# Kernel tuning notes

Measured on AMD Instinct MI355X. Metric: run time of the kernel, lower is better.

Reference implementation:

```python
import jax, jax.numpy as jnp
import numpy as np

N = 200_000
E = 6_400_000
EPS = 1e-12


def l2_normalize(x):
    # F.normalize(x, p=2, dim=1): x / max(||x||_2, eps)
    n = jnp.linalg.norm(x, axis=1, keepdims=True)
    return x / jnp.maximum(n, EPS)


def gcn_conv(x, W, b, src, dst, n):
    """PyG GCNConv: add self-loops, symmetric normalization D^-1/2 A D^-1/2,
    linear transform (no bias) on nodes, scatter-add to targets, then + bias."""
    loop = jnp.arange(n)
    s = jnp.concatenate([src, loop])  # sources (messages gathered here)
    d = jnp.concatenate([dst, loop])  # targets (aggregation here)
    deg = jax.ops.segment_sum(jnp.ones(s.shape[0], dtype=x.dtype), d, num_segments=n)
    dinv = jnp.where(deg > 0, jax.lax.rsqrt(deg), 0.0)
    norm = dinv[s] * dinv[d]  # [E+N]
    h = x @ W  # [N, out]
    out = jax.ops.segment_sum(norm[:, None] * h[s], d, num_segments=n)
    return out + b


def setup_inputs() -> dict:
    key = jax.random.key(0)
    ks = jax.random.split(key, 10)
    x = jax.random.normal(ks[0], (N, 3), dtype=jnp.float32)
    edge_index = jax.random.randint(ks[1], (2, E), 0, N, dtype=jnp.int64)

    def glorot(k, shape):
        lim = float(np.sqrt(6.0 / (shape[0] + shape[1])))
        return jax.random.uniform(k, shape, jnp.float32, -lim, lim)

    return {
        "x": x,
        "edge_index": edge_index,
        "W1": glorot(ks[2], (3, 6)),   "b1": jnp.zeros((6,), jnp.float32),
        "W2": glorot(ks[3], (6, 12)),  "b2": jnp.zeros((12,), jnp.float32),
        "W3": glorot(ks[4], (12, 24)), "b3": jnp.zeros((24,), jnp.float32),
        "Wc": glorot(ks[5], (24, 13)), "bc": jnp.zeros((13,), jnp.float32),
    }


def reference(x, edge_index, W1, b1, W2, b2, W3, b3, Wc, bc):
    src, dst = edge_index[0], edge_index[1]
    n = x.shape[0]
    h = jnp.tanh(gcn_conv(x, W1, b1, src, dst, n))
    h = jnp.tanh(l2_normalize(gcn_conv(h, W2, b2, src, dst, n)))
    h = l2_normalize(gcn_conv(h, W3, b3, src, dst, n))
    h = h @ Wc + bc
    return l2_normalize(h)
```

## Files before the change

### kernel.cpp

```cpp
#include <hip/hip_runtime.h>
#include <math.h>


static constexpr int NN = 200000;
static constexpr int NE = 6400000;
static constexpr int BK = 256;

static constexpr int SUBW  = 512;
static constexpr int NBA   = (NN + SUBW - 1) / SUBW;
static constexpr int CAP   = 32;
static constexpr int FLUSH = 16;
static constexpr int CAPB  = 18400;
static constexpr int BKP   = 512;
static constexpr int EPT   = 4;
static constexpr int CHUNK = BKP * EPT;
static constexpr int GPART = 768;
static constexpr int SRCSH = 13;
static constexpr int NSB   = (NN + (1 << SRCSH) - 1) >> SRCSH;

static constexpr int S     = 4;
static constexpr int LOGS  = 2;

__global__ void __launch_bounds__(BKP) k_part(const int* __restrict__ srcI,
                                              const int* __restrict__ dstI,
                                              unsigned* __restrict__ stg,
                                              int* __restrict__ gtail, int e) {
  __shared__ unsigned bin[CAP][NBA];
  __shared__ int bcnt[NBA];
  for (int t = threadIdx.x; t < NBA; t += BKP) bcnt[t] = 0;
  __syncthreads();
  int nchunks = (e + CHUNK - 1) / CHUNK;
  for (int c = blockIdx.x; c < nchunks; c += gridDim.x) {
    int base_i = c * CHUNK;
    int dv[EPT], sv[EPT];
#pragma unroll
    for (int u = 0; u < EPT; ++u) {
      int i = base_i + u * BKP + (int)threadIdx.x;
      dv[u] = (i < e) ? __builtin_nontemporal_load(dstI + i) : -1;
      sv[u] = (i < e) ? __builtin_nontemporal_load(srcI + i) : 0;
    }
#pragma unroll
    for (int u = 0; u < EPT; ++u) {
      if (dv[u] >= 0) {
        int b = dv[u] >> 9;
        unsigned rec = ((unsigned)(dv[u] & (SUBW - 1)) << 18) | (unsigned)sv[u];
        int p = atomicAdd(&bcnt[b], 1);
        if (p < CAP) {
          bin[p][b] = rec;
        } else {
          int base = atomicAdd(&gtail[b], 1);
          stg[(size_t)b * CAPB + base] = rec;
        }
      }
    }
    __syncthreads();
    int b2 = threadIdx.x;
    if (b2 < NBA) {
      int c2 = bcnt[b2];
      if (c2 > CAP) c2 = CAP;
      if (c2 >= FLUSH) {
        int nfl = c2 & ~(FLUSH - 1);
        int base = atomicAdd(&gtail[b2], nfl);
        size_t o = (size_t)b2 * CAPB + base;
        for (int k = 0; k < nfl; k += 4) {
          uint4 v;
          v.x = bin[k][b2]; v.y = bin[k + 1][b2]; v.z = bin[k + 2][b2]; v.w = bin[k + 3][b2];
          *(uint4*)(stg + o + k) = v;
        }
        int r = c2 - nfl;
        for (int k = 0; k < r; ++k) bin[k][b2] = bin[nfl + k][b2];
        bcnt[b2] = r;
      }
    }
    __syncthreads();
  }
  int b2 = threadIdx.x;
  if (b2 < NBA) {
    int c2 = bcnt[b2];
    if (c2 > CAP) c2 = CAP;
    if (c2 > 0) {
      int base = atomicAdd(&gtail[b2], c2);
      size_t o = (size_t)b2 * CAPB + base;
      for (int k = 0; k < c2; ++k) stg[o + k] = bin[k][b2];
    }
  }
}

__global__ void k_scan_sub(const int* __restrict__ gtail, int* __restrict__ sbase) {
  __shared__ int s0[512], s1[512];
  int t = threadIdx.x;
  int v = (t < NBA) ? gtail[t] : 0;
  s0[t] = v;
  __syncthreads();
  int* a = s0; int* b = s1;
  for (int off = 1; off < 512; off <<= 1) {
    int x = a[t] + ((t >= off) ? a[t - off] : 0);
    b[t] = x;
    __syncthreads();
    int* tmp = a; a = b; b = tmp;
  }
  if (t < NBA) sbase[t] = a[t] - v;
}

__global__ void __launch_bounds__(BK) k_build(const unsigned* __restrict__ stg,
                                              const int* __restrict__ gtail,
                                              const int* __restrict__ sbase,
                                              int* __restrict__ rowptr,
                                              int* __restrict__ adj,
                                              int* __restrict__ b7,
                                              int* __restrict__ b13,
                                              int* __restrict__ b19) {
  __shared__ unsigned hist2[SUBW * NSB];
  __shared__ int htot[SUBW];
  __shared__ int s0[SUBW], s1[SUBW];
  int b = blockIdx.x;
  int m = gtail[b]; if (m > CAPB) m = CAPB;
  size_t off = (size_t)b * CAPB;
  int base = sbase[b];
  if (b == NBA - 1 && threadIdx.x == 0) rowptr[NN] = base + m;
  for (int t = threadIdx.x; t < SUBW * NSB; t += BK) hist2[t] = 0;
  __syncthreads();
  for (int k = threadIdx.x; k < m; k += BK) {
    unsigned rec = stg[off + k];
    int dl = rec >> 18;
    int sb = (int)((rec & 0x3FFFFu) >> SRCSH);
    atomicAdd(&hist2[dl * NSB + sb], 1u);
  }
  __syncthreads();
  for (int dl = threadIdx.x; dl < SUBW; dl += BK) {
    unsigned run = 0;
    for (int sb = 0; sb < NSB; ++sb) {
      unsigned c = hist2[dl * NSB + sb];
      hist2[dl * NSB + sb] = run;
      run += c;
    }
    htot[dl] = (int)run;
    s0[dl] = (int)run;
  }
  __syncthreads();
  int* a = s0; int* bb = s1;
  for (int o2 = 1; o2 < SUBW; o2 <<= 1) {
    for (int t = threadIdx.x; t < SUBW; t += BK) bb[t] = a[t] + ((t >= o2) ? a[t - o2] : 0);
    __syncthreads();
    int* tmp = a; a = bb; bb = tmp;
  }
  for (int t = threadIdx.x; t < SUBW; t += BK) {
    int node = b * SUBW + t;
    int ex = a[t] - htot[t];
    if (node < NN) {
      rowptr[node] = base + ex;
      b7[node]  = base + ex + (int)hist2[t * NSB + 7];
      b13[node] = base + ex + (int)hist2[t * NSB + 13];
      b19[node] = base + ex + (int)hist2[t * NSB + 19];
    }
    bb[t] = ex;
  }
  __syncthreads();
  for (int k = threadIdx.x; k < m; k += BK) {
    unsigned rec = stg[off + k];
    int dl = rec >> 18;
    unsigned src = rec & 0x3FFFFu;
    int sb = (int)(src >> SRCSH);
    int p = bb[dl] + (int)atomicAdd(&hist2[dl * NSB + sb], 1u);
    adj[base + p] = (int)src;
  }
}

__global__ void k_zero(int* __restrict__ p, int n) {
  int i = blockIdx.x * blockDim.x + threadIdx.x;
  if (i < n) p[i] = 0;
}

__global__ void k_dinv(const int* __restrict__ rowptr, float* __restrict__ dinv, int n) {
  int i = blockIdx.x * blockDim.x + threadIdx.x;
  if (i < n) dinv[i] = rsqrtf(1.0f + (float)(rowptr[i + 1] - rowptr[i]));
}

__global__ void k_prep(const float* __restrict__ x, const float* __restrict__ dinv,
                       float* __restrict__ p1, int n) {
  int i = blockIdx.x * blockDim.x + threadIdx.x;
  if (i >= n) return;
  float di = dinv[i];
  float3 v;
  v.x = di * x[3 * (size_t)i];
  v.y = di * x[3 * (size_t)i + 1];
  v.z = di * x[3 * (size_t)i + 2];
  *(float3*)(p1 + 3 * (size_t)i) = v;
}

template <int RW> struct RowT;
template <> struct RowT<3> {
  using T = float3;
  static __device__ inline T ld(const float* __restrict__ p) { return *(const float3*)p; }
  static __device__ inline void add(float* __restrict__ a, const T& v) {
    a[0] += v.x; a[1] += v.y; a[2] += v.z;
  }
  static __device__ inline void st(float* __restrict__ p, const float* __restrict__ a) {
    *(float3*)p = make_float3(a[0], a[1], a[2]);
  }
};
template <> struct RowT<6> {
  struct T { float2 a, b, c; };
  static __device__ inline T ld(const float* __restrict__ p) {
    T t; t.a = *(const float2*)p; t.b = *(const float2*)(p + 2); t.c = *(const float2*)(p + 4);
    return t;
  }
  static __device__ inline void add(float* __restrict__ a, const T& v) {
    a[0] += v.a.x; a[1] += v.a.y; a[2] += v.b.x; a[3] += v.b.y; a[4] += v.c.x; a[5] += v.c.y;
  }
  static __device__ inline void st(float* __restrict__ p, const float* __restrict__ a) {
    *(float2*)(p)     = make_float2(a[0], a[1]);
    *(float2*)(p + 2) = make_float2(a[2], a[3]);
    *(float2*)(p + 4) = make_float2(a[4], a[5]);
  }
};
template <> struct RowT<12> {
  struct T { float4 a, b, c; };
  static __device__ inline T ld(const float* __restrict__ p) {
    T t; t.a = *(const float4*)p; t.b = *(const float4*)(p + 4); t.c = *(const float4*)(p + 8);
    return t;
  }
  static __device__ inline void add(float* __restrict__ a, const T& v) {
    a[0] += v.a.x; a[1] += v.a.y; a[2] += v.a.z; a[3] += v.a.w;
    a[4] += v.b.x; a[5] += v.b.y; a[6] += v.b.z; a[7] += v.b.w;
    a[8] += v.c.x; a[9] += v.c.y; a[10] += v.c.z; a[11] += v.c.w;
  }
  static __device__ inline void st(float* __restrict__ p, const float* __restrict__ a) {
    *(float4*)(p)     = make_float4(a[0], a[1], a[2], a[3]);
    *(float4*)(p + 4) = make_float4(a[4], a[5], a[6], a[7]);
    *(float4*)(p + 8) = make_float4(a[8], a[9], a[10], a[11]);
  }
};

template <int RW, int UN>
__device__ inline void gather_p(const int* __restrict__ adj, int st, int en,
                                const float* __restrict__ pin, float* __restrict__ acc,
                                int slot) {
  using RT = RowT<RW>;
  using T = typename RT::T;
  int k = st + slot;
  if (k + (UN - 1) * S < en) {
    int a[UN];
#pragma unroll
    for (int u = 0; u < UN; ++u) a[u] = adj[k + u * S];
    for (;;) {
      int kn = k + UN * S;
      bool more = (kn + (UN - 1) * S < en);
      int b[UN];
#pragma unroll
      for (int u = 0; u < UN; ++u) b[u] = 0;
      if (more) {
#pragma unroll
        for (int u = 0; u < UN; ++u) b[u] = adj[kn + u * S];
      }
      T v[UN];
#pragma unroll
      for (int u = 0; u < UN; ++u) v[u] = RT::ld(pin + (size_t)a[u] * RW);
#pragma unroll
      for (int u = 0; u < UN; ++u) RT::add(acc, v[u]);
      k = kn;
      if (!more) break;
#pragma unroll
      for (int u = 0; u < UN; ++u) a[u] = b[u];
    }
  }
  for (; k < en; k += S) {
    T v = RT::ld(pin + (size_t)adj[k] * RW);
    RT::add(acc, v);
  }
}

template <int FIN>
__device__ inline void group_reduce(float* __restrict__ acc) {
#pragma unroll
  for (int j = 0; j < FIN; ++j) {
    acc[j] += __shfl_xor(acc[j], 1);
    acc[j] += __shfl_xor(acc[j], 2);
  }
}

template <int RW, int FOUT, int MODE>
__global__ void __launch_bounds__(BK, 8) k_gather_fused(
    const int* __restrict__ adj, const int* __restrict__ rowptr,
    const float* __restrict__ pin, const float* __restrict__ W,
    const float* __restrict__ bias, const float* __restrict__ dinv,
    float* __restrict__ pout, int n) {
  __shared__ float sW[RW * FOUT];
  __shared__ float sb[FOUT];
  for (int t = threadIdx.x; t < RW * FOUT; t += BK) sW[t] = W[t];
  if (threadIdx.x < FOUT) sb[threadIdx.x] = bias[threadIdx.x];
  __syncthreads();
  int g = blockIdx.x * blockDim.x + threadIdx.x;
  int i = g >> LOGS;
  int slot = g & (S - 1);
  if (i >= n) return;
  float acc[RW] = {};
  if (slot == 0) {
    typename RowT<RW>::T v = RowT<RW>::ld(pin + (size_t)i * RW);
    RowT<RW>::add(acc, v);
  }
  gather_p<RW, 4>(adj, rowptr[i], rowptr[i + 1], pin, acc, slot);
  group_reduce<RW>(acc);
  float di = dinv[i];
  float h[FOUT];
  float ss = 0.f;
#pragma unroll
  for (int j = 0; j < FOUT; ++j) {
    float s = 0.f;
#pragma unroll
    for (int kk = 0; kk < RW; ++kk) s = fmaf(acc[kk], sW[kk * FOUT + j], s);
    float t = fmaf(di, s, sb[j]);
    h[j] = t;
    ss += t * t;
  }
  float o[FOUT];
  if (MODE == 0) {
#pragma unroll
    for (int j = 0; j < FOUT; ++j) o[j] = di * tanhf(h[j]);
  } else {
    float inv = 1.f / fmaxf(sqrtf(ss), 1e-12f);
#pragma unroll
    for (int j = 0; j < FOUT; ++j) o[j] = di * tanhf(h[j] * inv);
  }
  if (slot == 0) {
    float* po = pout + (size_t)i * FOUT;
    if (MODE == 0) {
      *(float2*)(po)     = make_float2(o[0], o[1]);
      *(float2*)(po + 2) = make_float2(o[2], o[3]);
      *(float2*)(po + 4) = make_float2(o[4], o[5]);
    } else {
      *(float4*)(po)     = make_float4(o[0], o[1], o[2], o[3]);
      *(float4*)(po + 4) = make_float4(o[4], o[5], o[6], o[7]);
      *(float4*)(po + 8) = make_float4(o[8], o[9], o[10], o[11]);
    }
  }
}

template <int RW, bool FIRST>
__global__ void __launch_bounds__(BK, 8) k_gphase(
    const int* __restrict__ adj, const int* __restrict__ stA,
    const int* __restrict__ enB, const float* __restrict__ pin,
    float* __restrict__ accb, int n) {
  int g = blockIdx.x * blockDim.x + threadIdx.x;
  int i = g >> LOGS;
  int slot = g & (S - 1);
  if (i >= n) return;
  float acc[RW] = {};
  if (slot == 0) {
    if (FIRST) {
      typename RowT<RW>::T v = RowT<RW>::ld(pin + (size_t)i * RW);
      RowT<RW>::add(acc, v);
    } else {
      typename RowT<RW>::T v = RowT<RW>::ld(accb + (size_t)i * RW);
      RowT<RW>::add(acc, v);
    }
  }
  gather_p<RW, 2>(adj, stA[i], enB[i], pin, acc, slot);
  group_reduce<RW>(acc);
  if (slot == 0) RowT<RW>::st(accb + (size_t)i * RW, acc);
}

template <int RW, int FOUT, int MODE>
__global__ void __launch_bounds__(BK, 6) k_gphase_last(
    const int* __restrict__ adj, const int* __restrict__ stA,
    const int* __restrict__ rowptr, const float* __restrict__ pin,
    const float* __restrict__ W, const float* __restrict__ bias,
    const float* __restrict__ Wc, const float* __restrict__ bc,
    const float* __restrict__ dinv, const float* __restrict__ accb,
    float* __restrict__ out, int n) {
  constexpr int FC = 13;
  __shared__ float sW[RW * FOUT];
  __shared__ float sb[FOUT];
  __shared__ float sWc[MODE == 2 ? FOUT * FC : 1];
  __shared__ float sbc[MODE == 2 ? FC : 1];
  for (int t = threadIdx.x; t < RW * FOUT; t += BK) sW[t] = W[t];
  if (threadIdx.x < FOUT) sb[threadIdx.x] = bias[threadIdx.x];
  if (MODE == 2) {
    for (int t = threadIdx.x; t < FOUT * FC; t += BK) sWc[t] = Wc[t];
    if (threadIdx.x < FC) sbc[threadIdx.x] = bc[threadIdx.x];
  }
  __syncthreads();
  int g = blockIdx.x * blockDim.x + threadIdx.x;
  int i = g >> LOGS;
  int slot = g & (S - 1);
  if (i >= n) return;
  float acc[RW] = {};
  if (slot == 0) {
    typename RowT<RW>::T v = RowT<RW>::ld(accb + (size_t)i * RW);
    RowT<RW>::add(acc, v);
  }
  gather_p<RW, 2>(adj, stA[i], rowptr[i + 1], pin, acc, slot);
  group_reduce<RW>(acc);
  float di = dinv[i];
  float h[FOUT];
  float ss = 0.f;
#pragma unroll
  for (int j = 0; j < FOUT; ++j) {
    float s = 0.f;
#pragma unroll
    for (int kk = 0; kk < RW; ++kk) s = fmaf(acc[kk], sW[kk * FOUT + j], s);
    float t = fmaf(di, s, sb[j]);
    h[j] = t;
    ss += t * t;
  }
  float inv = 1.f / fmaxf(sqrtf(ss), 1e-12f);
  if (MODE == 1) {
    float o[FOUT];
#pragma unroll
    for (int j = 0; j < FOUT; ++j) o[j] = di * tanhf(h[j] * inv);
    if (slot == 0) {
      float* po = out + (size_t)i * FOUT;
      *(float4*)(po)     = make_float4(o[0], o[1], o[2], o[3]);
      *(float4*)(po + 4) = make_float4(o[4], o[5], o[6], o[7]);
      *(float4*)(po + 8) = make_float4(o[8], o[9], o[10], o[11]);
    }
  } else {
    float v[FC];
    float ss2 = 0.f;
#pragma unroll
    for (int j = 0; j < FC; ++j) {
      float s = sbc[j];
#pragma unroll
      for (int kk = 0; kk < FOUT; ++kk) s = fmaf(h[kk] * inv, sWc[kk * FC + j], s);
      v[j] = s;
      ss2 += s * s;
    }
    float inv2 = 1.f / fmaxf(sqrtf(ss2), 1e-12f);
    if (slot == 0) {
#pragma unroll
      for (int j = 0; j < FC; ++j) out[(size_t)i * FC + j] = v[j] * inv2;
    }
  }
}

extern "C" void kernel_launch(void* const* d_in, const int* in_sizes, int n_in,
                              void* d_out, int out_size, void* d_ws, size_t ws_size,
                              hipStream_t stream) {
  const float* x  = (const float*)d_in[0];
  const int*   ei = (const int*)d_in[1];
  const float* W1 = (const float*)d_in[2];
  const float* b1 = (const float*)d_in[3];
  const float* W2 = (const float*)d_in[4];
  const float* b2 = (const float*)d_in[5];
  const float* W3 = (const float*)d_in[6];
  const float* b3 = (const float*)d_in[7];
  const float* Wc = (const float*)d_in[8];
  const float* bc = (const float*)d_in[9];
  float* out = (float*)d_out;

  const int n = NN;
  const int e = NE;
  const int* srcI = ei;
  const int* dstI = ei + e;

  float* ws = (float*)d_ws;
  float* dinv  = ws;
  int* rowptr  = (int*)(ws + n);
  int* gtail   = rowptr + n + 8;
  int* sbase   = gtail + 512;
  int* adj     = sbase + 512;
  int* b7      = adj + e;
  int* b13     = b7 + n;
  int* b19     = b13 + n;
  size_t roff = (size_t)n + (n + 8) + 512 + 512 + e + 3 * (size_t)n;
  roff = (roff + 15) & ~(size_t)15;
  float* R     = ws + roff;
  unsigned* stg = (unsigned*)R;
  float* p1   = R;
  float* p2   = R + (size_t)3 * n;
  float* p3   = R + (size_t)9 * n;
  float* accb = R + (size_t)21 * n;

  const int gn  = (n + BK - 1) / BK;
  const int gnS = (n * S + BK - 1) / BK;

  k_zero<<<2, BK, 0, stream>>>(gtail, 512);
  k_part<<<GPART, BKP, 0, stream>>>(srcI, dstI, stg, gtail, e);
  k_scan_sub<<<1, 512, 0, stream>>>(gtail, sbase);
  k_build<<<NBA, BK, 0, stream>>>(stg, gtail, sbase, rowptr, adj, b7, b13, b19);
  k_dinv<<<gn, BK, 0, stream>>>(rowptr, dinv, n);

  k_prep<<<gn, BK, 0, stream>>>(x, dinv, p1, n);

  k_gather_fused<3, 6, 0><<<gnS, BK, 0, stream>>>(adj, rowptr, p1, W1, b1, dinv, p2, n);

  k_gphase<6, true><<<gnS, BK, 0, stream>>>(adj, rowptr, b13, p2, accb, n);
  k_gphase_last<6, 12, 1><<<gnS, BK, 0, stream>>>(adj, b13, rowptr, p2, W2, b2,
                                                  Wc, bc, dinv, accb, p3, n);

  k_gphase<12, true><<<gnS, BK, 0, stream>>>(adj, rowptr, b7, p3, accb, n);
  k_gphase<12, false><<<gnS, BK, 0, stream>>>(adj, b7, b13, p3, accb, n);
  k_gphase<12, false><<<gnS, BK, 0, stream>>>(adj, b13, b19, p3, accb, n);
  k_gphase_last<12, 24, 2><<<gnS, BK, 0, stream>>>(adj, b19, rowptr, p3, W3, b3,
                                                   Wc, bc, dinv, accb, out, n);
}
```

Baseline: 461.0 us.

## Build CSR via global atomic histogram, scan, and scatter with source quarters

Replaces the LDS-binned partition/build CSR construction with a counting-sort path: a global atomic histogram keyed by (dst, source quarter), a three-kernel prefix scan, and an atomic-cursor scatter into adj. The per-node quarter boundaries replace the separate b7/b13/b19 arrays, so the phased gather kernels read start/end from one interleaved ebase array. This drops the staging buffer and the per-bucket local sort, but the scatter writes become uncoalesced and order within a (node, quarter) segment is nondeterministic. Adjacency loads in the gather loops are also made nontemporal.

```diff
diff --git a/kernel.cpp b/kernel.cpp
--- a/kernel.cpp
+++ b/kernel.cpp
@@ -6,163 +6,140 @@
 static constexpr int NE = 6400000;
 static constexpr int BK = 256;
 
-static constexpr int SUBW  = 512;
-static constexpr int NBA   = (NN + SUBW - 1) / SUBW;
-static constexpr int CAP   = 32;
-static constexpr int FLUSH = 16;
-static constexpr int CAPB  = 18400;
-static constexpr int BKP   = 512;
-static constexpr int EPT   = 4;
-static constexpr int CHUNK = BKP * EPT;
-static constexpr int GPART = 768;
-static constexpr int SRCSH = 13;
-static constexpr int NSB   = (NN + (1 << SRCSH) - 1) >> SRCSH;
-
-static constexpr int S     = 4;
-static constexpr int LOGS  = 2;
-
-__global__ void __launch_bounds__(BKP) k_part(const int* __restrict__ srcI,
+static constexpr int QDIV = NN / 4;
+static constexpr int SCT  = 4096;
+
+static constexpr int S    = 4;
+static constexpr int LOGS = 2;
+
+__global__ void __launch_bounds__(256) k_hist(const int* __restrict__ srcI,
                                               const int* __restrict__ dstI,
-                                              unsigned* __restrict__ stg,
-                                              int* __restrict__ gtail, int e) {
-  __shared__ unsigned bin[CAP][NBA];
-  __shared__ int bcnt[NBA];
-  for (int t = threadIdx.x; t < NBA; t += BKP) bcnt[t] = 0;
+                                              int* __restrict__ cnt, int e) {
+  int T = gridDim.x * blockDim.x;
+  int i0 = blockIdx.x * blockDim.x + threadIdx.x;
+#pragma unroll
+  for (int u = 0; u < 8; ++u) {
+    int i = i0 + u * T;
+    if (i < e) {
+      int s = __builtin_nontemporal_load(srcI + i);
+      int d = __builtin_nontemporal_load(dstI + i);
+      int qp = (int)((unsigned)s / (unsigned)QDIV);
+      atomicAdd(&cnt[4 * d + qp], 1);
+    }
+  }
+}
+
+__global__ void __launch_bounds__(256) k_scan1(const int* __restrict__ cnt,
+                                               int* __restrict__ bsum, int M) {
+  __shared__ int red[256];
+  int b = blockIdx.x, t = threadIdx.x;
+  int base = b * SCT + t * 16;
+  int s = 0;
+  if (base + 16 <= M) {
+    const uint4* p = (const uint4*)(cnt + base);
+#pragma unroll
+    for (int j = 0; j < 4; ++j) { uint4 v = p[j]; s += (int)(v.x + v.y + v.z + v.w); }
+  } else {
+    for (int j = 0; j < 16; ++j) if (base + j < M) s += cnt[base + j];
+  }
+  red[t] = s;
   __syncthreads();
-  int nchunks = (e + CHUNK - 1) / CHUNK;
-  for (int c = blockIdx.x; c < nchunks; c += gridDim.x) {
-    int base_i = c * CHUNK;
-    int dv[EPT], sv[EPT];
-#pragma unroll
-    for (int u = 0; u < EPT; ++u) {
-      int i = base_i + u * BKP + (int)threadIdx.x;
-      dv[u] = (i < e) ? __builtin_nontemporal_load(dstI + i) : -1;
-      sv[u] = (i < e) ? __builtin_nontemporal_load(srcI + i) : 0;
-    }
-#pragma unroll
-    for (int u = 0; u < EPT; ++u) {
-      if (dv[u] >= 0) {
-        int b = dv[u] >> 9;
-        unsigned rec = ((unsigned)(dv[u] & (SUBW - 1)) << 18) | (unsigned)sv[u];
-        int p = atomicAdd(&bcnt[b], 1);
-        if (p < CAP) {
-          bin[p][b] = rec;
-        } else {
-          int base = atomicAdd(&gtail[b], 1);
-          stg[(size_t)b * CAPB + base] = rec;
-        }
-      }
-    }
+  for (int o = 128; o > 0; o >>= 1) {
+    if (t < o) red[t] += red[t + o];
     __syncthreads();
-    int b2 = threadIdx.x;
-    if (b2 < NBA) {
-      int c2 = bcnt[b2];
-      if (c2 > CAP) c2 = CAP;
-      if (c2 >= FLUSH) {
-        int nfl = c2 & ~(FLUSH - 1);
-        int base = atomicAdd(&gtail[b2], nfl);
-        size_t o = (size_t)b2 * CAPB + base;
-        for (int k = 0; k < nfl; k += 4) {
-          uint4 v;
-          v.x = bin[k][b2]; v.y = bin[k + 1][b2]; v.z = bin[k + 2][b2]; v.w = bin[k + 3][b2];
-          *(uint4*)(stg + o + k) = v;
-        }
-        int r = c2 - nfl;
-        for (int k = 0; k < r; ++k) bin[k][b2] = bin[nfl + k][b2];
-        bcnt[b2] = r;
-      }
-    }
-    __syncthreads();
-  }
-  int b2 = threadIdx.x;
-  if (b2 < NBA) {
-    int c2 = bcnt[b2];
-    if (c2 > CAP) c2 = CAP;
-    if (c2 > 0) {
-      int base = atomicAdd(&gtail[b2], c2);
-      size_t o = (size_t)b2 * CAPB + base;
-      for (int k = 0; k < c2; ++k) stg[o + k] = bin[k][b2];
-    }
-  }
-}
-
-__global__ void k_scan_sub(const int* __restrict__ gtail, int* __restrict__ sbase) {
-  __shared__ int s0[512], s1[512];
+  }
+  if (t == 0) bsum[b] = red[0];
+}
+
+__global__ void k_scan2(int* __restrict__ bsum, int* __restrict__ ebase,
+                        int nbl, int M) {
+  __shared__ int s0[256], s1[256];
   int t = threadIdx.x;
-  int v = (t < NBA) ? gtail[t] : 0;
+  int v = (t < nbl) ? bsum[t] : 0;
   s0[t] = v;
   __syncthreads();
   int* a = s0; int* b = s1;
-  for (int off = 1; off < 512; off <<= 1) {
-    int x = a[t] + ((t >= off) ? a[t - off] : 0);
-    b[t] = x;
+  for (int o = 1; o < 256; o <<= 1) {
+    b[t] = a[t] + ((t >= o) ? a[t - o] : 0);
     __syncthreads();
     int* tmp = a; a = b; b = tmp;
   }
-  if (t < NBA) sbase[t] = a[t] - v;
-}
-
-__global__ void __launch_bounds__(BK) k_build(const unsigned* __restrict__ stg,
-                                              const int* __restrict__ gtail,
-                                              const int* __restrict__ sbase,
-                                              int* __restrict__ rowptr,
-                                              int* __restrict__ adj,
-                                              int* __restrict__ b7,
-                                              int* __restrict__ b13,
-                                              int* __restrict__ b19) {
-  __shared__ unsigned hist2[SUBW * NSB];
-  __shared__ int htot[SUBW];
-  __shared__ int s0[SUBW], s1[SUBW];
-  int b = blockIdx.x;
-  int m = gtail[b]; if (m > CAPB) m = CAPB;
-  size_t off = (size_t)b * CAPB;
-  int base = sbase[b];
-  if (b == NBA - 1 && threadIdx.x == 0) rowptr[NN] = base + m;
-  for (int t = threadIdx.x; t < SUBW * NSB; t += BK) hist2[t] = 0;
-  __syncthreads();
-  for (int k = threadIdx.x; k < m; k += BK) {
-    unsigned rec = stg[off + k];
-    int dl = rec >> 18;
-    int sb = (int)((rec & 0x3FFFFu) >> SRCSH);
-    atomicAdd(&hist2[dl * NSB + sb], 1u);
-  }
-  __syncthreads();
-  for (int dl = threadIdx.x; dl < SUBW; dl += BK) {
-    unsigned run = 0;
-    for (int sb = 0; sb < NSB; ++sb) {
-      unsigned c = hist2[dl * NSB + sb];
-      hist2[dl * NSB + sb] = run;
-      run += c;
-    }
-    htot[dl] = (int)run;
-    s0[dl] = (int)run;
-  }
+  if (t < nbl) bsum[t] = a[t] - v;
+  if (t == nbl - 1) ebase[M] = a[t];
+}
+
+__global__ void __launch_bounds__(256) k_scan3(const int* __restrict__ cnt,
+                                               const int* __restrict__ bsum,
+                                               int* __restrict__ ebase,
+                                               int* __restrict__ cursor, int M) {
+  __shared__ int s0[256], s1[256];
+  int b = blockIdx.x, t = threadIdx.x;
+  int base = b * SCT + t * 16;
+  int loc[16];
+  int s = 0;
+  if (base + 16 <= M) {
+    const uint4* p = (const uint4*)(cnt + base);
+#pragma unroll
+    for (int j = 0; j < 4; ++j) {
+      uint4 v = p[j];
+      loc[4 * j]     = s; s += (int)v.x;
+      loc[4 * j + 1] = s; s += (int)v.y;
+      loc[4 * j + 2] = s; s += (int)v.z;
+      loc[4 * j + 3] = s; s += (int)v.w;
+    }
+  } else {
+    for (int j = 0; j < 16; ++j) {
+      loc[j] = s;
+      if (base + j < M) s += cnt[base + j];
+    }
+  }
+  s0[t] = s;
   __syncthreads();
   int* a = s0; int* bb = s1;
-  for (int o2 = 1; o2 < SUBW; o2 <<= 1) {
-    for (int t = threadIdx.x; t < SUBW; t += BK) bb[t] = a[t] + ((t >= o2) ? a[t - o2] : 0);
+  for (int o = 1; o < 256; o <<= 1) {
+    bb[t] = a[t] + ((t >= o) ? a[t - o] : 0);
     __syncthreads();
     int* tmp = a; a = bb; bb = tmp;
   }
-  for (int t = threadIdx.x; t < SUBW; t += BK) {
-    int node = b * SUBW + t;
-    int ex = a[t] - htot[t];
-    if (node < NN) {
-      rowptr[node] = base + ex;
-      b7[node]  = base + ex + (int)hist2[t * NSB + 7];
-      b13[node] = base + ex + (int)hist2[t * NSB + 13];
-      b19[node] = base + ex + (int)hist2[t * NSB + 19];
-    }
-    bb[t] = ex;
-  }
-  __syncthreads();
-  for (int k = threadIdx.x; k < m; k += BK) {
-    unsigned rec = stg[off + k];
-    int dl = rec >> 18;
-    unsigned src = rec & 0x3FFFFu;
-    int sb = (int)(src >> SRCSH);
-    int p = bb[dl] + (int)atomicAdd(&hist2[dl * NSB + sb], 1u);
-    adj[base + p] = (int)src;
+  int off = bsum[b] + a[t] - s;
+  if (base + 16 <= M) {
+    uint4* pe = (uint4*)(ebase + base);
+    uint4* pc = (uint4*)(cursor + base);
+#pragma unroll
+    for (int j = 0; j < 4; ++j) {
+      uint4 v;
+      v.x = (unsigned)(off + loc[4 * j]);
+      v.y = (unsigned)(off + loc[4 * j + 1]);
+      v.z = (unsigned)(off + loc[4 * j + 2]);
+      v.w = (unsigned)(off + loc[4 * j + 3]);
+      pe[j] = v; pc[j] = v;
+    }
+  } else {
+    for (int j = 0; j < 16; ++j) {
+      if (base + j < M) {
+        ebase[base + j] = off + loc[j];
+        cursor[base + j] = off + loc[j];
+      }
+    }
+  }
+}
+
+__global__ void __launch_bounds__(256) k_scatter(const int* __restrict__ srcI,
+                                                 const int* __restrict__ dstI,
+                                                 int* __restrict__ cursor,
+                                                 int* __restrict__ adj, int e) {
+  int T = gridDim.x * blockDim.x;
+  int i0 = blockIdx.x * blockDim.x + threadIdx.x;
+#pragma unroll
+  for (int u = 0; u < 8; ++u) {
+    int i = i0 + u * T;
+    if (i < e) {
+      int s = __builtin_nontemporal_load(srcI + i);
+      int d = __builtin_nontemporal_load(dstI + i);
+      int qp = (int)((unsigned)s / (unsigned)QDIV);
+      int pos = atomicAdd(&cursor[4 * d + qp], 1);
+      adj[pos] = s;
+    }
   }
 }
 
@@ -171,9 +148,9 @@
   if (i < n) p[i] = 0;
 }
 
-__global__ void k_dinv(const int* __restrict__ rowptr, float* __restrict__ dinv, int n) {
+__global__ void k_dinv(const int* __restrict__ eb, float* __restrict__ dinv, int n) {
   int i = blockIdx.x * blockDim.x + threadIdx.x;
-  if (i < n) dinv[i] = rsqrtf(1.0f + (float)(rowptr[i + 1] - rowptr[i]));
+  if (i < n) dinv[i] = rsqrtf(1.0f + (float)(eb[4 * i + 4] - eb[4 * i]));
 }
 
 __global__ void k_prep(const float* __restrict__ x, const float* __restrict__ dinv,
@@ -242,7 +219,7 @@
   if (k + (UN - 1) * S < en) {
     int a[UN];
 #pragma unroll
-    for (int u = 0; u < UN; ++u) a[u] = adj[k + u * S];
+    for (int u = 0; u < UN; ++u) a[u] = __builtin_nontemporal_load(adj + k + u * S);
     for (;;) {
       int kn = k + UN * S;
       bool more = (kn + (UN - 1) * S < en);
@@ -251,7 +228,7 @@
       for (int u = 0; u < UN; ++u) b[u] = 0;
       if (more) {
 #pragma unroll
-        for (int u = 0; u < UN; ++u) b[u] = adj[kn + u * S];
+        for (int u = 0; u < UN; ++u) b[u] = __builtin_nontemporal_load(adj + kn + u * S);
       }
       T v[UN];
 #pragma unroll
@@ -265,7 +242,7 @@
     }
   }
   for (; k < en; k += S) {
-    T v = RT::ld(pin + (size_t)adj[k] * RW);
+    T v = RT::ld(pin + (size_t)__builtin_nontemporal_load(adj + k) * RW);
     RT::add(acc, v);
   }
 }
@@ -281,7 +258,7 @@
 
 template <int RW, int FOUT, int MODE>
 __global__ void __launch_bounds__(BK, 8) k_gather_fused(
-    const int* __restrict__ adj, const int* __restrict__ rowptr,
+    const int* __restrict__ adj, const int* __restrict__ eb,
     const float* __restrict__ pin, const float* __restrict__ W,
     const float* __restrict__ bias, const float* __restrict__ dinv,
     float* __restrict__ pout, int n) {
@@ -299,7 +276,7 @@
     typename RowT<RW>::T v = RowT<RW>::ld(pin + (size_t)i * RW);
     RowT<RW>::add(acc, v);
   }
-  gather_p<RW, 4>(adj, rowptr[i], rowptr[i + 1], pin, acc, slot);
+  gather_p<RW, 4>(adj, eb[4 * i], eb[4 * i + 4], pin, acc, slot);
   group_reduce<RW>(acc);
   float di = dinv[i];
   float h[FOUT];
@@ -336,11 +313,10 @@
   }
 }
 
-template <int RW, bool FIRST>
+template <int RW, bool FIRST, int OA, int OB>
 __global__ void __launch_bounds__(BK, 8) k_gphase(
-    const int* __restrict__ adj, const int* __restrict__ stA,
-    const int* __restrict__ enB, const float* __restrict__ pin,
-    float* __restrict__ accb, int n) {
+    const int* __restrict__ adj, const int* __restrict__ eb,
+    const float* __restrict__ pin, float* __restrict__ accb, int n) {
   int g = blockIdx.x * blockDim.x + threadIdx.x;
   int i = g >> LOGS;
   int slot = g & (S - 1);
@@ -355,19 +331,18 @@
       RowT<RW>::add(acc, v);
     }
   }
-  gather_p<RW, 2>(adj, stA[i], enB[i], pin, acc, slot);
+  gather_p<RW, 2>(adj, eb[4 * i + OA], eb[4 * i + OB], pin, acc, slot);
   group_reduce<RW>(acc);
   if (slot == 0) RowT<RW>::st(accb + (size_t)i * RW, acc);
 }
 
-template <int RW, int FOUT, int MODE>
+template <int RW, int FOUT, int MODE, int OA>
 __global__ void __launch_bounds__(BK, 6) k_gphase_last(
-    const int* __restrict__ adj, const int* __restrict__ stA,
-    const int* __restrict__ rowptr, const float* __restrict__ pin,
-    const float* __restrict__ W, const float* __restrict__ bias,
-    const float* __restrict__ Wc, const float* __restrict__ bc,
-    const float* __restrict__ dinv, const float* __restrict__ accb,
-    float* __restrict__ out, int n) {
+    const int* __restrict__ adj, const int* __restrict__ eb,
+    const float* __restrict__ pin, const float* __restrict__ W,
+    const float* __restrict__ bias, const float* __restrict__ Wc,
+    const float* __restrict__ bc, const float* __restrict__ dinv,
+    const float* __restrict__ accb, float* __restrict__ out, int n) {
   constexpr int FC = 13;
   __shared__ float sW[RW * FOUT];
   __shared__ float sb[FOUT];
@@ -389,7 +364,7 @@
     typename RowT<RW>::T v = RowT<RW>::ld(accb + (size_t)i * RW);
     RowT<RW>::add(acc, v);
   }
-  gather_p<RW, 2>(adj, stA[i], rowptr[i + 1], pin, acc, slot);
+  gather_p<RW, 2>(adj, eb[4 * i + OA], eb[4 * i + 4], pin, acc, slot);
   group_reduce<RW>(acc);
   float di = dinv[i];
   float h[FOUT];
@@ -450,22 +425,20 @@
 
   const int n = NN;
   const int e = NE;
+  const int M = 4 * n;
   const int* srcI = ei;
   const int* dstI = ei + e;
 
   float* ws = (float*)d_ws;
   float* dinv  = ws;
-  int* rowptr  = (int*)(ws + n);
-  int* gtail   = rowptr + n + 8;
-  int* sbase   = gtail + 512;
-  int* adj     = sbase + 512;
-  int* b7      = adj + e;
-  int* b13     = b7 + n;
-  int* b19     = b13 + n;
-  size_t roff = (size_t)n + (n + 8) + 512 + 512 + e + 3 * (size_t)n;
+  int* ebase   = (int*)(ws + n);
+  int* cnt     = ebase + M + 4;
+  int* cursor  = cnt + M;
+  int* bsum    = cursor + M;
+  int* adj     = bsum + 256;
+  size_t roff = (size_t)n + (M + 4) + M + M + 256 + e;
   roff = (roff + 15) & ~(size_t)15;
   float* R     = ws + roff;
-  unsigned* stg = (unsigned*)R;
   float* p1   = R;
   float* p2   = R + (size_t)3 * n;
   float* p3   = R + (size_t)9 * n;
@@ -473,24 +446,28 @@
 
   const int gn  = (n + BK - 1) / BK;
   const int gnS = (n * S + BK - 1) / BK;
-
-  k_zero<<<2, BK, 0, stream>>>(gtail, 512);
-  k_part<<<GPART, BKP, 0, stream>>>(srcI, dstI, stg, gtail, e);
-  k_scan_sub<<<1, 512, 0, stream>>>(gtail, sbase);
-  k_build<<<NBA, BK, 0, stream>>>(stg, gtail, sbase, rowptr, adj, b7, b13, b19);
-  k_dinv<<<gn, BK, 0, stream>>>(rowptr, dinv, n);
+  const int gE  = (e + 256 * 8 - 1) / (256 * 8);
+  const int NBL = (M + SCT - 1) / SCT;
+
+  k_zero<<<(M + 255) / 256, 256, 0, stream>>>(cnt, M);
+  k_hist<<<gE, 256, 0, stream>>>(srcI, dstI, cnt, e);
+  k_scan1<<<NBL, 256, 0, stream>>>(cnt, bsum, M);
+  k_scan2<<<1, 256, 0, stream>>>(bsum, ebase, NBL, M);
+  k_scan3<<<NBL, 256, 0, stream>>>(cnt, bsum, ebase, cursor, M);
+  k_scatter<<<gE, 256, 0, stream>>>(srcI, dstI, cursor, adj, e);
+  k_dinv<<<gn, BK, 0, stream>>>(ebase, dinv, n);
 
   k_prep<<<gn, BK, 0, stream>>>(x, dinv, p1, n);
 
-  k_gather_fused<3, 6, 0><<<gnS, BK, 0, stream>>>(adj, rowptr, p1, W1, b1, dinv, p2, n);
-
-  k_gphase<6, true><<<gnS, BK, 0, stream>>>(adj, rowptr, b13, p2, accb, n);
-  k_gphase_last<6, 12, 1><<<gnS, BK, 0, stream>>>(adj, b13, rowptr, p2, W2, b2,
-                                                  Wc, bc, dinv, accb, p3, n);
-
-  k_gphase<12, true><<<gnS, BK, 0, stream>>>(adj, rowptr, b7, p3, accb, n);
-  k_gphase<12, false><<<gnS, BK, 0, stream>>>(adj, b7, b13, p3, accb, n);
-  k_gphase<12, false><<<gnS, BK, 0, stream>>>(adj, b13, b19, p3, accb, n);
-  k_gphase_last<12, 24, 2><<<gnS, BK, 0, stream>>>(adj, b19, rowptr, p3, W3, b3,
-                                                   Wc, bc, dinv, accb, out, n);
-}
+  k_gather_fused<3, 6, 0><<<gnS, BK, 0, stream>>>(adj, ebase, p1, W1, b1, dinv, p2, n);
+
+  k_gphase<6, true, 0, 2><<<gnS, BK, 0, stream>>>(adj, ebase, p2, accb, n);
+  k_gphase_last<6, 12, 1, 2><<<gnS, BK, 0, stream>>>(adj, ebase, p2, W2, b2,
+                                                     Wc, bc, dinv, accb, p3, n);
+
+  k_gphase<12, true, 0, 1><<<gnS, BK, 0, stream>>>(adj, ebase, p3, accb, n);
+  k_gphase<12, false, 1, 2><<<gnS, BK, 0, stream>>>(adj, ebase, p3, accb, n);
+  k_gphase<12, false, 2, 3><<<gnS, BK, 0, stream>>>(adj, ebase, p3, accb, n);
+  k_gphase_last<12, 24, 2, 3><<<gnS, BK, 0, stream>>>(adj, ebase, p3, W3, b3,
+                                                      Wc, bc, dinv, accb, out, n);
+}
```

Result: slower. 1.040 ms (+125.5%).
